# Kernel tuning notes

Measured on AMD Instinct MI355X. Metric: run time of the kernel, lower is better.

The kernel has to match this reference:

```python
import jax, jax.numpy as jnp
import numpy as np

D, NQ, BS, NL, NH, NP, DFF = 256, 900, 8, 4, 8, 4, 1024
HD = D // NH
SHAPES = np.array([[100, 100], [50, 50], [25, 25], [13, 13]], dtype=np.int64)  # (H, W) per level
LSTART = np.concatenate([[0], np.cumsum(SHAPES[:, 0] * SHAPES[:, 1])[:-1]]).astype(np.int64)
LMEM = int((SHAPES[:, 0] * SHAPES[:, 1]).sum())


def layer_norm(x, g, b, eps=1e-5):
    mu = x.mean(-1, keepdims=True)
    var = ((x - mu) ** 2).mean(-1, keepdims=True)
    return (x - mu) * jax.lax.rsqrt(var + eps) * g + b


def _forward(tgt, tgt_query_pos, tgt_reference_points, memory,
             in_proj_w, in_proj_b, out_proj_w, out_proj_b,
             samp_off_w, samp_off_b, attn_w_w, attn_w_b,
             value_proj_w, value_proj_b, output_proj_w, output_proj_b,
             lin1_w, lin1_b, lin2_w, lin2_b,
             norm1_g, norm1_b, norm2_g, norm2_b, norm3_g, norm3_b):
    # ---- self-attention (seq-first, torch nn.MultiheadAttention semantics) ----
    q = tgt + tgt_query_pos  # q = k = with_pos_embed(tgt, pos)
    Wq, Wk, Wv = jnp.split(in_proj_w, 3, 0)
    bq, bk, bv = jnp.split(in_proj_b, 3, 0)
    def heads(x):  # (nq, bs, d) -> (bs, nh, nq, hd)
        return x.reshape(NQ, BS, NH, HD).transpose(1, 2, 0, 3)
    qh = heads(q @ Wq.T + bq)
    kh = heads(q @ Wk.T + bk)
    vh = heads(tgt @ Wv.T + bv)
    attn = jax.nn.softmax(jnp.einsum('bhqd,bhkd->bhqk', qh, kh) / np.float32(np.sqrt(HD)), -1)
    sa = jnp.einsum('bhqk,bhkd->bhqd', attn, vh).transpose(2, 0, 1, 3).reshape(NQ, BS, D)
    sa = sa @ out_proj_w.T + out_proj_b
    t = layer_norm(tgt + sa, norm2_g, norm2_b)

    # ---- MSDeformAttn cross-attention (batch-first internally) ----
    qb = (t + tgt_query_pos).transpose(1, 0, 2)          # (bs, nq, d)
    refb = tgt_reference_points.transpose(1, 0, 2, 3)    # (bs, nq, nl, 2) in [0,1]
    memb = memory.transpose(1, 0, 2)                     # (bs, L, d)
    value = (memb @ value_proj_w.T + value_proj_b).reshape(BS, LMEM, NH, HD)
    off = (qb @ samp_off_w.T + samp_off_b).reshape(BS, NQ, NH, NL, NP, 2)
    aw = jax.nn.softmax((qb @ attn_w_w.T + attn_w_b).reshape(BS, NQ, NH, NL * NP), -1)
    aw = aw.reshape(BS, NQ, NH, NL, NP)
    normz = jnp.asarray(SHAPES[:, ::-1].copy(), dtype=jnp.float32)  # (nl, 2) = [W, H]
    loc = refb[:, :, None, :, None, :] + off / normz[None, None, None, :, None, :]

    out = jnp.zeros((BS, NQ, NH, HD), jnp.float32)
    for l in range(NL):  # fixed small number of pyramid levels
        Hl, Wl = int(SHAPES[l, 0]), int(SHAPES[l, 1])
        s = int(LSTART[l])
        v_l = value[:, s:s + Hl * Wl]  # (bs, Hl*Wl, nh, hd)
        # grid_sample(align_corners=False, padding=zeros) pixel coords
        x = (loc[:, :, :, l, :, 0] * Wl - 0.5).transpose(0, 1, 3, 2).reshape(BS, NQ * NP, NH)
        y = (loc[:, :, :, l, :, 1] * Hl - 0.5).transpose(0, 1, 3, 2).reshape(BS, NQ * NP, NH)
        x0 = jnp.floor(x)
        y0 = jnp.floor(y)
        samp = jnp.zeros((BS, NQ * NP, NH, HD), jnp.float32)
        for dx in (0, 1):
            for dy in (0, 1):
                xc = x0 + dx
                yc = y0 + dy
                w = (1.0 - jnp.abs(x - xc)) * (1.0 - jnp.abs(y - yc))
                valid = (xc >= 0) & (xc < Wl) & (yc >= 0) & (yc < Hl)
                idx = (jnp.clip(yc, 0, Hl - 1) * Wl + jnp.clip(xc, 0, Wl - 1)).astype(jnp.int32)
                g = jnp.take_along_axis(v_l, idx[..., None], axis=1)  # (bs, nq*np, nh, hd)
                samp = samp + jnp.where(valid, w, 0.0)[..., None] * g
        samp = samp.reshape(BS, NQ, NP, NH, HD)
        out = out + jnp.einsum('bqhp,bqphd->bqhd', aw[:, :, :, l], samp)
    ca = (out.reshape(BS, NQ, D) @ output_proj_w.T + output_proj_b).transpose(1, 0, 2)
    t = layer_norm(t + ca, norm1_g, norm1_b)

    # ---- FFN ----
    ffn = jax.nn.relu(t @ lin1_w.T + lin1_b) @ lin2_w.T + lin2_b
    return layer_norm(t + ffn, norm3_g, norm3_b)


def setup_inputs() -> dict:
    key = jax.random.key(0)
    ks = jax.random.split(key, 24)
    r = lambda i, shape, s: jax.random.normal(ks[i], shape, jnp.float32) * s
    return {
        'tgt': r(0, (NQ, BS, D), 1.0),
        'tgt_query_pos': r(1, (NQ, BS, D), 1.0),
        'tgt_reference_points': jax.random.uniform(ks[2], (NQ, BS, NL, 2), jnp.float32),
        'memory': r(3, (LMEM, BS, D), 1.0),
        'spatial_shapes': jnp.asarray(SHAPES),
        'level_start_index': jnp.asarray(LSTART),
        'in_proj_w': r(4, (3 * D, D), 0.02), 'in_proj_b': r(5, (3 * D,), 0.02),
        'out_proj_w': r(6, (D, D), 0.02), 'out_proj_b': r(7, (D,), 0.02),
        'samp_off_w': r(8, (NH * NL * NP * 2, D), 0.01), 'samp_off_b': r(9, (NH * NL * NP * 2,), 0.01),
        'attn_w_w': r(10, (NH * NL * NP, D), 0.02), 'attn_w_b': r(11, (NH * NL * NP,), 0.02),
        'value_proj_w': r(12, (D, D), 0.02), 'value_proj_b': r(13, (D,), 0.02),
        'output_proj_w': r(14, (D, D), 0.02), 'output_proj_b': r(15, (D,), 0.02),
        'lin1_w': r(16, (DFF, D), 0.02), 'lin1_b': r(17, (DFF,), 0.02),
        'lin2_w': r(18, (D, DFF), 0.02), 'lin2_b': r(19, (D,), 0.02),
        'norm1_g': jnp.ones((D,), jnp.float32), 'norm1_b': jnp.zeros((D,), jnp.float32),
        'norm2_g': jnp.ones((D,), jnp.float32), 'norm2_b': jnp.zeros((D,), jnp.float32),
        'norm3_g': jnp.ones((D,), jnp.float32), 'norm3_b': jnp.zeros((D,), jnp.float32),
    }


def reference(tgt, tgt_query_pos, tgt_reference_points, memory, spatial_shapes, level_start_index,
              in_proj_w, in_proj_b, out_proj_w, out_proj_b, samp_off_w, samp_off_b,
              attn_w_w, attn_w_b, value_proj_w, value_proj_b, output_proj_w, output_proj_b,
              lin1_w, lin1_b, lin2_w, lin2_b, norm1_g, norm1_b, norm2_g, norm2_b, norm3_g, norm3_b):
    # spatial_shapes / level_start_index are static level constants (module-level SHAPES/LSTART)
    return _forward(tgt, tgt_query_pos, tgt_reference_points, memory,
                    in_proj_w, in_proj_b, out_proj_w, out_proj_b,
                    samp_off_w, samp_off_b, attn_w_w, attn_w_b,
                    value_proj_w, value_proj_b, output_proj_w, output_proj_b,
                    lin1_w, lin1_b, lin2_w, lin2_b,
                    norm1_g, norm1_b, norm2_g, norm2_b, norm3_g, norm3_b)
```

## Files before the change

kernel.cpp:

```cpp
#include <hip/hip_runtime.h>
#include <hip/hip_bf16.h>


namespace {
constexpr int D_ = 256;
constexpr int NQ_ = 900;
constexpr int BS_ = 8;
constexpr int NH_ = 8;
constexpr int HD_ = 32;
constexpr int DFF_ = 1024;
constexpr int MTOK = NQ_ * BS_;
constexpr int LMEM_ = 13294;
constexpr long T = (long)MTOK * D_;
constexpr float QSC = 0.17677669529663687f;
constexpr int QKS = 512;
constexpr int MVAL = BS_ * LMEM_;
}

typedef __attribute__((ext_vector_type(8))) short bf8_t;
typedef __attribute__((ext_vector_type(4))) float f4_t;

#define MFMA16(a, b, c) __builtin_amdgcn_mfma_f32_16x16x32_bf16((a), (b), (c), 0, 0, 0)

__device__ __forceinline__ unsigned short bfbits(float x) {
    union { __hip_bfloat16 h; unsigned short u; } cv;
    cv.h = __float2bfloat16(x);
    return cv.u;
}
__device__ __forceinline__ float bf2f(unsigned short u) {
    union { float f; unsigned v; } cv;
    cv.v = ((unsigned)u) << 16;
    return cv.f;
}

__device__ __forceinline__ void gload16(const unsigned short* g, unsigned short* l) {
    __builtin_amdgcn_global_load_lds(
        (const __attribute__((address_space(1))) unsigned int*)(g),
        (__attribute__((address_space(3))) unsigned int*)(l), 16, 0, 0);
}
__device__ __forceinline__ void gload16f(const float* g, float* l) {
    __builtin_amdgcn_global_load_lds(
        (const __attribute__((address_space(1))) unsigned int*)(g),
        (__attribute__((address_space(3))) unsigned int*)(l), 16, 0, 0);
}

__global__ void conv_weights(
    const float* __restrict__ ipw, const float* __restrict__ opw,
    const float* __restrict__ sow, const float* __restrict__ aww,
    const float* __restrict__ vpw, const float* __restrict__ outpw,
    const float* __restrict__ l1w, const float* __restrict__ l2w,
    const float* __restrict__ ipb, const float* __restrict__ sob,
    const float* __restrict__ awb,
    unsigned short* __restrict__ Wbf, float* __restrict__ biasAll)
{
    if (blockIdx.x == 0) {
        for (int j = threadIdx.x; j < 512; j += 256)
            biasAll[j] = (j < 256) ? ipb[j] * QSC : ipb[j];
        for (int j = threadIdx.x; j < 384; j += 256)
            biasAll[512 + j] = (j < 256) ? sob[j] : awb[j - 256];
    }
    const long idx4 = (long)blockIdx.x * 256 + threadIdx.x;
    if (idx4 >= 253952) return;
    const long e = idx4 * 4;
    const float* src; long off; float sc = 1.f;
    if (e < 196608)      { src = ipw;   off = 0;      if (e < 65536) sc = QSC; }
    else if (e < 262144) { src = opw;   off = 196608; }
    else if (e < 327680) { src = sow;   off = 262144; }
    else if (e < 360448) { src = aww;   off = 327680; }
    else if (e < 425984) { src = vpw;   off = 360448; }
    else if (e < 491520) { src = outpw; off = 425984; }
    else if (e < 753664) { src = l1w;   off = 491520; }
    else                 { src = l2w;   off = 753664; }
    const float4 v = *(const float4*)(src + (e - off));
    union { unsigned short u[4]; uint2 w; } pk;
    pk.u[0] = bfbits(v.x * sc); pk.u[1] = bfbits(v.y * sc);
    pk.u[2] = bfbits(v.z * sc); pk.u[3] = bfbits(v.w * sc);
    *(uint2*)(Wbf + e) = pk.w;
}

template<bool RELU, bool OUTBF16>
__global__ __launch_bounds__(256) void gemm_mfma(
    const unsigned short* __restrict__ A, const unsigned short* __restrict__ W,
    const float* __restrict__ bias, void* __restrict__ C, int M, int N, int K)
{
    __shared__ unsigned short As[128 * 32];
    __shared__ unsigned short Ws[128 * 32];
    const int t = threadIdx.x;
    const long m0 = (long)blockIdx.x * 128;
    const int n0 = blockIdx.y * 128;
    const int row0 = t >> 2;
    const int cgp = (t & 3) ^ ((t >> 2) & 3);
    long ar0 = m0 + row0;        if (ar0 > M - 1) ar0 = M - 1;
    long ar1 = m0 + 64 + row0;   if (ar1 > M - 1) ar1 = M - 1;
    const unsigned short* ga0 = A + ar0 * K + cgp * 8;
    const unsigned short* ga1 = A + ar1 * K + cgp * 8;
    const unsigned short* gw0 = W + (long)(n0 + row0) * K + cgp * 8;
    const unsigned short* gw1 = W + (long)(n0 + 64 + row0) * K + cgp * 8;
    const int lane = t & 63, wave = t >> 6;
    const int c = lane & 15, g = lane >> 4;
    const int wr = wave >> 1, wc = wave & 1;
    const int sws = (g * 8) ^ ((c & 3) * 8);
    f4_t acc[4][4];
#pragma unroll
    for (int i = 0; i < 4; ++i)
#pragma unroll
        for (int j = 0; j < 4; ++j)
            acc[i][j] = f4_t{0.f, 0.f, 0.f, 0.f};

    for (int kb = 0; kb < K; kb += 32) {
        gload16(ga0 + kb, As + t * 8);
        gload16(ga1 + kb, As + 2048 + t * 8);
        gload16(gw0 + kb, Ws + t * 8);
        gload16(gw1 + kb, Ws + 2048 + t * 8);
        __syncthreads();
        bf8_t af[4], bfr[4];
#pragma unroll
        for (int i = 0; i < 4; ++i) {
            af[i] = *(const bf8_t*)(As + (wr * 64 + i * 16 + c) * 32 + sws);
            bfr[i] = *(const bf8_t*)(Ws + (wc * 64 + i * 16 + c) * 32 + sws);
        }
#pragma unroll
        for (int i = 0; i < 4; ++i)
#pragma unroll
            for (int j = 0; j < 4; ++j)
                acc[i][j] = MFMA16(af[i], bfr[j], acc[i][j]);
        __syncthreads();
    }

#pragma unroll
    for (int i = 0; i < 4; ++i) {
        const long rbase = m0 + wr * 64 + i * 16 + 4 * g;
#pragma unroll
        for (int j = 0; j < 4; ++j) {
            const int col = n0 + wc * 64 + j * 16 + c;
            const float bv = bias[col];
#pragma unroll
            for (int r = 0; r < 4; ++r) {
                const long rr = rbase + r;
                if (rr < M) {
                    float v = acc[i][j][r] + bv;
                    if (RELU) v = fmaxf(v, 0.f);
                    if (OUTBF16) ((unsigned short*)C)[rr * N + col] = bfbits(v);
                    else         ((float*)C)[rr * N + col] = v;
                }
            }
        }
    }
}

template<bool OUTBF16>
__global__ __launch_bounds__(256) void gemm_f32d(
    const float* __restrict__ A, const unsigned short* __restrict__ W,
    const float* __restrict__ bias, void* __restrict__ C,
    int M, int N, int K)
{
    __shared__ float Asf[64 * 64];
    __shared__ unsigned short Ws[128 * 64];
    const int t = threadIdx.x;
    const long m0 = (long)blockIdx.x * 64;
    const int n0 = blockIdx.y * 128;
    const float* gA[4];
#pragma unroll
    for (int l = 0; l < 4; ++l) {
        int r = (int)m0 + l * 16 + (t >> 4); if (r > M - 1) r = M - 1;
        const int sp = (t & 15) ^ ((t >> 4) & 15);
        gA[l] = A + (long)r * K + sp * 4;
    }
    const unsigned short* gW[4];
#pragma unroll
    for (int l = 0; l < 4; ++l) {
        const int r = l * 32 + (t >> 3);
        const int sp = (t & 7) ^ (r & 7);
        gW[l] = W + (long)(n0 + r) * K + sp * 8;
    }
    const int lane = t & 63, wave = t >> 6;
    const int c = lane & 15, g = lane >> 4;
    const int wr = wave >> 1, wc = wave & 1;
    f4_t acc[2][4];
#pragma unroll
    for (int i = 0; i < 2; ++i)
#pragma unroll
        for (int j = 0; j < 4; ++j)
            acc[i][j] = f4_t{0.f, 0.f, 0.f, 0.f};

    for (int kb = 0; kb < K; kb += 64) {
#pragma unroll
        for (int l = 0; l < 4; ++l) gload16f(gA[l] + kb, Asf + l * 1024 + t * 4);
#pragma unroll
        for (int l = 0; l < 4; ++l) gload16(gW[l] + kb, Ws + l * 2048 + t * 8);
        __syncthreads();
#pragma unroll
        for (int s = 0; s < 2; ++s) {
            bf8_t af[2], bfr[4];
#pragma unroll
            for (int i = 0; i < 2; ++i) {
                const int row = wr * 32 + i * 16 + c;
                const int sl0 = (s * 8 + 2 * g) ^ (row & 15);
                const int sl1 = (s * 8 + 2 * g + 1) ^ (row & 15);
                const f4_t lo = *(const f4_t*)(Asf + row * 64 + sl0 * 4);
                const f4_t hi = *(const f4_t*)(Asf + row * 64 + sl1 * 4);
                union { bf8_t v; unsigned short u[8]; } pk;
                pk.u[0] = bfbits(lo[0]); pk.u[1] = bfbits(lo[1]);
                pk.u[2] = bfbits(lo[2]); pk.u[3] = bfbits(lo[3]);
                pk.u[4] = bfbits(hi[0]); pk.u[5] = bfbits(hi[1]);
                pk.u[6] = bfbits(hi[2]); pk.u[7] = bfbits(hi[3]);
                af[i] = pk.v;
            }
#pragma unroll
            for (int j = 0; j < 4; ++j) {
                const int row = wc * 64 + j * 16 + c;
                const int sl = (s * 4 + g) ^ (row & 7);
                bfr[j] = *(const bf8_t*)(Ws + row * 64 + sl * 8);
            }
#pragma unroll
            for (int i = 0; i < 2; ++i)
#pragma unroll
                for (int j = 0; j < 4; ++j)
                    acc[i][j] = MFMA16(af[i], bfr[j], acc[i][j]);
        }
        __syncthreads();
    }

#pragma unroll
    for (int i = 0; i < 2; ++i) {
        const long rbase = m0 + wr * 32 + i * 16 + 4 * g;
#pragma unroll
        for (int j = 0; j < 4; ++j) {
            const int col = n0 + wc * 64 + j * 16 + c;
            const float bv = bias[col];
#pragma unroll
            for (int r = 0; r < 4; ++r) {
                const long rr = rbase + r;
                if (rr < M) {
                    float v = acc[i][j][r] + bv;
                    if (OUTBF16) ((unsigned short*)C)[rr * N + col] = bfbits(v);
                    else         ((float*)C)[rr * N + col] = v;
                }
            }
        }
    }
}

template<bool OUTBF16>
__global__ __launch_bounds__(256) void gemm_f32a(
    const float* __restrict__ A, const float* __restrict__ A2,
    const unsigned short* __restrict__ W, const float* __restrict__ bias,
    void* __restrict__ C, int M, int N, int K)
{
    __shared__ unsigned short As[128 * 32];
    __shared__ unsigned short Ws[128 * 32];
    const int t = threadIdx.x;
    const long m0 = (long)blockIdx.x * 128;
    const int n0 = blockIdx.y * 128;
    const int row0 = t >> 2, cg = t & 3;
    const int cgp = cg ^ ((t >> 2) & 3);
    long ar0 = m0 + row0;        if (ar0 > M - 1) ar0 = M - 1;
    long ar1 = m0 + 64 + row0;   if (ar1 > M - 1) ar1 = M - 1;
    const float* Ap0 = A + ar0 * K + cg * 8;
    const float* Ap1 = A + ar1 * K + cg * 8;
    const float* Bp0 = A2 + ar0 * K + cg * 8;
    const float* Bp1 = A2 + ar1 * K + cg * 8;
    const unsigned short* gw0 = W + (long)(n0 + row0) * K + cgp * 8;
    const unsigned short* gw1 = W + (long)(n0 + 64 + row0) * K + cgp * 8;
    unsigned short* la0 = As + row0 * 32 + ((cg * 8) ^ ((row0 & 3) * 8));
    unsigned short* la1 = la0 + 2048;
    const int lane = t & 63, wave = t >> 6;
    const int c = lane & 15, g = lane >> 4;
    const int wr = wave >> 1, wc = wave & 1;
    const int sws = (g * 8) ^ ((c & 3) * 8);
    f4_t acc[4][4];
#pragma unroll
    for (int i = 0; i < 4; ++i)
#pragma unroll
        for (int j = 0; j < 4; ++j)
            acc[i][j] = f4_t{0.f, 0.f, 0.f, 0.f};

    for (int kb = 0; kb < K; kb += 32) {
        gload16(gw0 + kb, Ws + t * 8);
        gload16(gw1 + kb, Ws + 2048 + t * 8);
        const float4 a00 = *(const float4*)(Ap0 + kb);
        const float4 a01 = *(const float4*)(Ap0 + kb + 4);
        const float4 a10 = *(const float4*)(Ap1 + kb);
        const float4 a11 = *(const float4*)(Ap1 + kb + 4);
        const float4 b00 = *(const float4*)(Bp0 + kb);
        const float4 b01 = *(const float4*)(Bp0 + kb + 4);
        const float4 b10 = *(const float4*)(Bp1 + kb);
        const float4 b11 = *(const float4*)(Bp1 + kb + 4);
        union { bf8_t v; unsigned short u[8]; } p0, p1;
        p0.u[0] = bfbits(a00.x + b00.x); p0.u[1] = bfbits(a00.y + b00.y);
        p0.u[2] = bfbits(a00.z + b00.z); p0.u[3] = bfbits(a00.w + b00.w);
        p0.u[4] = bfbits(a01.x + b01.x); p0.u[5] = bfbits(a01.y + b01.y);
        p0.u[6] = bfbits(a01.z + b01.z); p0.u[7] = bfbits(a01.w + b01.w);
        p1.u[0] = bfbits(a10.x + b10.x); p1.u[1] = bfbits(a10.y + b10.y);
        p1.u[2] = bfbits(a10.z + b10.z); p1.u[3] = bfbits(a10.w + b10.w);
        p1.u[4] = bfbits(a11.x + b11.x); p1.u[5] = bfbits(a11.y + b11.y);
        p1.u[6] = bfbits(a11.z + b11.z); p1.u[7] = bfbits(a11.w + b11.w);
        *(bf8_t*)la0 = p0.v;
        *(bf8_t*)la1 = p1.v;
        __syncthreads();
        bf8_t af[4], bfr[4];
#pragma unroll
        for (int i = 0; i < 4; ++i) {
            af[i] = *(const bf8_t*)(As + (wr * 64 + i * 16 + c) * 32 + sws);
            bfr[i] = *(const bf8_t*)(Ws + (wc * 64 + i * 16 + c) * 32 + sws);
        }
#pragma unroll
        for (int i = 0; i < 4; ++i)
#pragma unroll
            for (int j = 0; j < 4; ++j)
                acc[i][j] = MFMA16(af[i], bfr[j], acc[i][j]);
        __syncthreads();
    }

#pragma unroll
    for (int i = 0; i < 4; ++i) {
        const long rbase = m0 + wr * 64 + i * 16 + 4 * g;
#pragma unroll
        for (int j = 0; j < 4; ++j) {
            const int col = n0 + wc * 64 + j * 16 + c;
            const float bv = bias[col];
#pragma unroll
            for (int r = 0; r < 4; ++r) {
                const long rr = rbase + r;
                if (rr < M) {
                    float v = acc[i][j][r] + bv;
                    if (OUTBF16) ((unsigned short*)C)[rr * N + col] = bfbits(v);
                    else         ((float*)C)[rr * N + col] = v;
                }
            }
        }
    }
}

__global__ __launch_bounds__(256) void attn_mfma(
    const unsigned short* __restrict__ Qb, const unsigned short* __restrict__ Kb,
    const unsigned short* __restrict__ Vb, unsigned short* __restrict__ sa)
{
    __shared__ float smemf[2112];
    unsigned short* Ks = (unsigned short*)smemf;
    unsigned short* Vt = (unsigned short*)(smemf + 1024);
    const int t = threadIdx.x;
    const int wave = t >> 6, lane = t & 63;
    const int g = lane >> 4, c = lane & 15;
    const int b = blockIdx.x >> 3, h = blockIdx.x & 7;
    const int q0 = blockIdx.y * 64 + wave * 16;
    const int q = q0 + c;
    const bool qv = q < NQ_;
    const bf8_t qf = *(const bf8_t*)(Qb + ((long)(qv ? q : 0) * BS_ + b) * QKS + h * HD_ + 8 * g);

    f4_t acc0 = {0.f, 0.f, 0.f, 0.f}, acc1 = {0.f, 0.f, 0.f, 0.f};
    float m_run = -1e30f, l_run = 0.f;
    const int sk = t >> 2, sd = (t & 3) * 8;

    for (int kc = 0; kc < NQ_; kc += 64) {
        __syncthreads();
        {
            const int key = kc + sk;
            union { bf8_t v; unsigned short u[8]; } kv, vv;
            if (key < NQ_) {
                kv.v = *(const bf8_t*)(Kb + ((long)key * BS_ + b) * QKS + h * HD_ + sd);
                vv.v = *(const bf8_t*)(Vb + ((long)key * BS_ + b) * D_ + h * HD_ + sd);
            } else {
#pragma unroll
                for (int u = 0; u < 8; ++u) { kv.u[u] = 0; vv.u[u] = 0; }
            }
            *(bf8_t*)(Ks + sk * 32 + sd) = kv.v;
#pragma unroll
            for (int u = 0; u < 8; ++u) {
                const int r = sd + u;
                Vt[r * 64 + (sk ^ ((r & 7) << 3))] = vv.u[u];
            }
        }
        __syncthreads();

        f4_t s[4];
#pragma unroll
        for (int tt = 0; tt < 4; ++tt) {
            const bf8_t kf = *(const bf8_t*)(Ks + (tt * 16 + c) * 32 + 8 * g);
            f4_t z = {0.f, 0.f, 0.f, 0.f};
            s[tt] = MFMA16(kf, qf, z);
        }
        float sv[16];
#pragma unroll
        for (int tt = 0; tt < 4; ++tt)
#pragma unroll
            for (int r = 0; r < 4; ++r) {
                float x = s[tt][r];
                if (kc + tt * 16 + 4 * g + r >= NQ_) x = -1e30f;
                sv[tt * 4 + r] = x;
            }
        float mloc = sv[0];
#pragma unroll
        for (int i = 1; i < 16; ++i) mloc = fmaxf(mloc, sv[i]);
        mloc = fmaxf(mloc, __shfl_xor(mloc, 16));
        mloc = fmaxf(mloc, __shfl_xor(mloc, 32));
        const float mnew = fmaxf(m_run, mloc);
        const float resc = __expf(m_run - mnew);
        float p[16], ls = 0.f;
#pragma unroll
        for (int i = 0; i < 16; ++i) { p[i] = __expf(sv[i] - mnew); ls += p[i]; }
        ls += __shfl_xor(ls, 16);
        ls += __shfl_xor(ls, 32);
        l_run = l_run * resc + ls;
        m_run = mnew;
#pragma unroll
        for (int r = 0; r < 4; ++r) { acc0[r] *= resc; acc1[r] *= resc; }

        unsigned pk[4][2];
#pragma unroll
        for (int tt = 0; tt < 4; ++tt) {
            pk[tt][0] = (unsigned)bfbits(p[tt * 4 + 0]) | ((unsigned)bfbits(p[tt * 4 + 1]) << 16);
            pk[tt][1] = (unsigned)bfbits(p[tt * 4 + 2]) | ((unsigned)bfbits(p[tt * 4 + 3]) << 16);
        }
        const int srcA = ((g & 1) << 5) + c;
        const int srcB = srcA + 16;
#pragma unroll
        for (int kh = 0; kh < 2; ++kh) {
            const unsigned a0 = __shfl(pk[kh * 2][0], srcA), b0_ = __shfl(pk[kh * 2 + 1][0], srcA);
            const unsigned a1 = __shfl(pk[kh * 2][1], srcA), b1_ = __shfl(pk[kh * 2 + 1][1], srcA);
            const unsigned a2 = __shfl(pk[kh * 2][0], srcB), b2_ = __shfl(pk[kh * 2 + 1][0], srcB);
            const unsigned a3 = __shfl(pk[kh * 2][1], srcB), b3_ = __shfl(pk[kh * 2 + 1][1], srcB);
            union { bf8_t v; unsigned u[4]; } pf;
            const bool hi = (g & 2);
            pf.u[0] = hi ? b0_ : a0; pf.u[1] = hi ? b1_ : a1;
            pf.u[2] = hi ? b2_ : a2; pf.u[3] = hi ? b3_ : a3;
            const int kcol = (kh * 32 + 8 * g) ^ ((c & 7) << 3);
            const bf8_t vf0 = *(const bf8_t*)(Vt + c * 64 + kcol);
            const bf8_t vf1 = *(const bf8_t*)(Vt + (16 + c) * 64 + kcol);
            acc0 = MFMA16(vf0, pf.v, acc0);
            acc1 = MFMA16(vf1, pf.v, acc1);
        }
    }

    __syncthreads();
    const float invl = 1.f / l_run;
    float* O = smemf + wave * 528;
#pragma unroll
    for (int r = 0; r < 4; ++r) {
        O[c * 33 + 4 * g + r] = acc0[r] * invl;
        O[c * 33 + 16 + 4 * g + r] = acc1[r] * invl;
    }
    __syncthreads();
    {
        const int ql = lane >> 2, part = lane & 3;
        const int qg = q0 + ql;
        if (qg < NQ_) {
            union { bf8_t v; unsigned short u[8]; } pk;
#pragma unroll
            for (int u = 0; u < 8; ++u) pk.u[u] = bfbits(O[ql * 33 + part * 8 + u]);
            *(bf8_t*)(sa + ((long)qg * BS_ + b) * D_ + h * HD_ + part * 8) = pk.v;
        }
    }
}

__global__ __launch_bounds__(256) void msdeform_kernel(
    const float* __restrict__ oa, const float* __restrict__ refp,
    const unsigned short* __restrict__ val, unsigned short* __restrict__ out)
{
    __shared__ float saw[128];
    __shared__ float redm[8], redi[8];
    __shared__ float swt[128][4];
    __shared__ int sidx[128][4];
    const int bq = blockIdx.x;
    const int b = bq / NQ_, q = bq % NQ_;
    const int t = threadIdx.x;
    if (t < 128) saw[t] = oa[(long)bq * 384 + 256 + t];
    __syncthreads();
    if (t < 8) {
        float mx = -1e30f;
        for (int i = 0; i < 16; ++i) mx = fmaxf(mx, saw[t * 16 + i]);
        float s = 0.f;
        for (int i = 0; i < 16; ++i) s += __expf(saw[t * 16 + i] - mx);
        redm[t] = mx; redi[t] = 1.f / s;
    }
    __syncthreads();
    if (t < 128) {
        const int h = t >> 4, lp = t & 15, l = lp >> 2, p = lp & 3;
        const float aw = __expf(saw[t] - redm[h]) * redi[h];
        const int Wi = (l == 0) ? 100 : (l == 1) ? 50 : (l == 2) ? 25 : 13;
        const int Hi = Wi;
        const int sl = (l == 0) ? 0 : (l == 1) ? 10000 : (l == 2) ? 12500 : 13125;
        const float offx = oa[(long)bq * 384 + h * 32 + l * 8 + p * 2 + 0];
        const float offy = oa[(long)bq * 384 + h * 32 + l * 8 + p * 2 + 1];
        const float refx = refp[(((long)q * BS_ + b) * 4 + l) * 2 + 0];
        const float refy = refp[(((long)q * BS_ + b) * 4 + l) * 2 + 1];
        const float fW = (float)Wi, fH = (float)Hi;
        const float x = (refx + offx / fW) * fW - 0.5f;
        const float y = (refy + offy / fH) * fH - 0.5f;
        const float x0f = floorf(x), y0f = floorf(y);
        const float fx = x - x0f, fy = y - y0f;
        const int ix = (int)x0f, iy = (int)y0f;
        const float wts[4] = {(1.f - fx) * (1.f - fy), fx * (1.f - fy),
                              (1.f - fx) * fy,          fx * fy};
        const int xs[4] = {ix, ix + 1, ix, ix + 1};
        const int ys[4] = {iy, iy, iy + 1, iy + 1};
#pragma unroll
        for (int tap = 0; tap < 4; ++tap) {
            const bool valid = (xs[tap] >= 0) & (xs[tap] < Wi) & (ys[tap] >= 0) & (ys[tap] < Hi);
            const int xc = min(max(xs[tap], 0), Wi - 1);
            const int yc = min(max(ys[tap], 0), Hi - 1);
            swt[t][tap] = valid ? aw * wts[tap] : 0.f;
            sidx[t][tap] = ((sl + yc * Wi + xc) << 3) + b;
        }
    }
    __syncthreads();
    const int h = t >> 5, r = t & 31, qd = r & 7, s = r >> 3;
    float a0 = 0.f, a1 = 0.f, a2 = 0.f, a3 = 0.f;
#pragma unroll
    for (int i = 0; i < 16; ++i) {
        const int j = h * 16 + i;
        const float wv = swt[j][s];
        const long base = (long)sidx[j][s] * D_ + h * HD_ + qd * 4;
        const uint2 raw = *(const uint2*)(val + base);
        a0 += wv * bf2f((unsigned short)(raw.x & 0xffff));
        a1 += wv * bf2f((unsigned short)(raw.x >> 16));
        a2 += wv * bf2f((unsigned short)(raw.y & 0xffff));
        a3 += wv * bf2f((unsigned short)(raw.y >> 16));
    }
    a0 += __shfl_xor(a0, 8); a0 += __shfl_xor(a0, 16);
    a1 += __shfl_xor(a1, 8); a1 += __shfl_xor(a1, 16);
    a2 += __shfl_xor(a2, 8); a2 += __shfl_xor(a2, 16);
    a3 += __shfl_xor(a3, 8); a3 += __shfl_xor(a3, 16);
    if (s == 0) {
        union { unsigned short u[4]; uint2 w; } pk;
        pk.u[0] = bfbits(a0); pk.u[1] = bfbits(a1); pk.u[2] = bfbits(a2); pk.u[3] = bfbits(a3);
        *(uint2*)(out + (long)bq * D_ + h * HD_ + qd * 4) = pk.w;
    }
}

__global__ __launch_bounds__(256) void ln_kernel(
    const float* __restrict__ inA, const float* __restrict__ inB,
    const float* __restrict__ g, const float* __restrict__ be,
    float* __restrict__ out, const float* __restrict__ pos,
    unsigned short* __restrict__ bfOut, int swapB, int bfMode)
{
    const int r = blockIdx.x * 4 + (threadIdx.x >> 6);
    const int lane = threadIdx.x & 63;
    long rb = r;
    if (swapB) rb = (long)(r & 7) * NQ_ + (r >> 3);
    const float4 a4 = *(const float4*)(inA + (long)r * D_ + lane * 4);
    const float4 b4 = *(const float4*)(inB + rb * D_ + lane * 4);
    float x[4] = {a4.x + b4.x, a4.y + b4.y, a4.z + b4.z, a4.w + b4.w};
    float s = x[0] + x[1] + x[2] + x[3];
#pragma unroll
    for (int off = 32; off > 0; off >>= 1) s += __shfl_xor(s, off);
    const float mu = s * (1.f / D_);
    float v = 0.f;
#pragma unroll
    for (int cc = 0; cc < 4; ++cc) { const float dd = x[cc] - mu; v += dd * dd; }
#pragma unroll
    for (int off = 32; off > 0; off >>= 1) v += __shfl_xor(v, off);
    const float rs = rsqrtf(v * (1.f / D_) + 1e-5f);
    const float4 g4 = *(const float4*)(g + lane * 4);
    const float4 e4 = *(const float4*)(be + lane * 4);
    const float gg[4] = {g4.x, g4.y, g4.z, g4.w};
    const float ee[4] = {e4.x, e4.y, e4.z, e4.w};
    float y[4];
#pragma unroll
    for (int cc = 0; cc < 4; ++cc) y[cc] = (x[cc] - mu) * rs * gg[cc] + ee[cc];
    *(float4*)(out + (long)r * D_ + lane * 4) = make_float4(y[0], y[1], y[2], y[3]);
    if (bfMode) {
        float z[4] = {y[0], y[1], y[2], y[3]};
        long er = r;
        if (bfMode == 2) {
            const float4 p4 = *(const float4*)(pos + (long)r * D_ + lane * 4);
            z[0] += p4.x; z[1] += p4.y; z[2] += p4.z; z[3] += p4.w;
            er = (long)(r & 7) * NQ_ + (r >> 3);
        }
        union { unsigned short u[4]; uint2 w; } pk;
        pk.u[0] = bfbits(z[0]); pk.u[1] = bfbits(z[1]);
        pk.u[2] = bfbits(z[2]); pk.u[3] = bfbits(z[3]);
        *(uint2*)(bfOut + er * D_ + lane * 4) = pk.w;
    }
}

extern "C" void kernel_launch(void* const* d_in, const int* in_sizes, int n_in,
                              void* d_out, int out_size, void* d_ws, size_t ws_size,
                              hipStream_t stream) {
    const float* tgt   = (const float*)d_in[0];
    const float* pos   = (const float*)d_in[1];
    const float* refp  = (const float*)d_in[2];
    const float* mem   = (const float*)d_in[3];
    const float* ipw   = (const float*)d_in[6];
    const float* ipb   = (const float*)d_in[7];
    const float* opw   = (const float*)d_in[8];
    const float* opb   = (const float*)d_in[9];
    const float* sow   = (const float*)d_in[10];
    const float* sob   = (const float*)d_in[11];
    const float* aww   = (const float*)d_in[12];
    const float* awb   = (const float*)d_in[13];
    const float* vpw   = (const float*)d_in[14];
    const float* vpb   = (const float*)d_in[15];
    const float* outpw = (const float*)d_in[16];
    const float* outpb = (const float*)d_in[17];
    const float* l1w   = (const float*)d_in[18];
    const float* l1b   = (const float*)d_in[19];
    const float* l2w   = (const float*)d_in[20];
    const float* l2b   = (const float*)d_in[21];
    const float* n1g = (const float*)d_in[22]; const float* n1be = (const float*)d_in[23];
    const float* n2g = (const float*)d_in[24]; const float* n2be = (const float*)d_in[25];
    const float* n3g = (const float*)d_in[26]; const float* n3be = (const float*)d_in[27];

    char* wsb = (char*)d_ws;
    auto alloc = [&](size_t bytes) { char* p = wsb; wsb += (bytes + 255) & ~(size_t)255; return p; };
    unsigned short* Wbf       = (unsigned short*)alloc(1015808 * 2);
    float*          biasAll   = (float*)alloc(896 * 4);
    unsigned short* QK_bf     = (unsigned short*)alloc(T * 4);
    unsigned short* Vb_bf     = (unsigned short*)alloc(T * 2);
    unsigned short* sa_bf     = (unsigned short*)alloc(T * 2);
    float*          saproj    = (float*)alloc(T * 4);
    float*          t1        = (float*)alloc(T * 4);
    unsigned short* qplus2_bf = (unsigned short*)alloc(T * 2);
    float*          oa        = (float*)alloc((long)MTOK * 384 * 4);
    unsigned short* sampo_bf  = (unsigned short*)alloc(T * 2);
    float*          ca        = (float*)alloc(T * 4);
    float*          t2        = (float*)alloc(T * 4);
    unsigned short* t2_bf     = (unsigned short*)alloc(T * 2);
    unsigned short* ffnh_bf   = (unsigned short*)alloc((long)MTOK * DFF_ * 2);
    float*          ffno      = (float*)alloc(T * 4);
    unsigned short* val       = (unsigned short*)alloc((long)MVAL * D_ * 2);
    const unsigned short* wqk   = Wbf + 0;
    const unsigned short* wv    = Wbf + 131072;
    const unsigned short* wo    = Wbf + 196608;
    const unsigned short* wsoaw = Wbf + 262144;
    const unsigned short* wvp   = Wbf + 360448;
    const unsigned short* wop   = Wbf + 425984;
    const unsigned short* wl1   = Wbf + 491520;
    const unsigned short* wl2   = Wbf + 753664;
    const float* bias_qk = biasAll;
    const float* bias_oa = biasAll + 512;

    const dim3 blk(256);
    const dim3 g_m(57, 2);

    conv_weights<<<992, blk, 0, stream>>>(ipw, opw, sow, aww, vpw, outpw, l1w, l2w,
                                          ipb, sob, awb, Wbf, biasAll);
    gemm_f32a<true><<<dim3(57, 4), blk, 0, stream>>>(tgt, pos, wqk, bias_qk, QK_bf,
                                                     MTOK, QKS, D_);
    gemm_f32d<true><<<dim3(113, 2), blk, 0, stream>>>(tgt, wv, ipb + 2 * D_, Vb_bf,
                                                      MTOK, D_, D_);
    attn_mfma<<<dim3(64, 15), blk, 0, stream>>>(QK_bf, QK_bf + 256, Vb_bf, sa_bf);
    gemm_mfma<false, false><<<g_m, blk, 0, stream>>>(sa_bf, wo, opb, saproj, MTOK, D_, D_);
    ln_kernel<<<1800, blk, 0, stream>>>(tgt, saproj, n2g, n2be, t1, pos, qplus2_bf, 0, 2);
    gemm_f32d<true><<<dim3(1662, 2), blk, 0, stream>>>(mem, wvp, vpb, val,
                                                       MVAL, D_, D_);
    gemm_mfma<false, false><<<dim3(57, 3), blk, 0, stream>>>(qplus2_bf, wsoaw, bias_oa, oa, MTOK, 384, D_);
    msdeform_kernel<<<7200, blk, 0, stream>>>(oa, refp, val, sampo_bf);
    gemm_mfma<false, false><<<g_m, blk, 0, stream>>>(sampo_bf, wop, outpb, ca, MTOK, D_, D_);
    ln_kernel<<<1800, blk, 0, stream>>>(t1, ca, n1g, n1be, t2, nullptr, t2_bf, 1, 1);
    gemm_mfma<true, true><<<dim3(57, 8), blk, 0, stream>>>(t2_bf, wl1, l1b, ffnh_bf, MTOK, DFF_, D_);
    gemm_mfma<false, false><<<g_m, blk, 0, stream>>>(ffnh_bf, wl2, l2b, ffno, MTOK, D_, DFF_);
    ln_kernel<<<1800, blk, 0, stream>>>(t2, ffno, n3g, n3be, (float*)d_out, nullptr, nullptr, 0, 0);
}
```

Measured before the change: 251.1 us.

## Fuse QKV projection into one GEMM and use persistent value-proj GEMM

The Q/K and V in-projections now run as one GEMM over a 768-wide output. A per-block flag skips the pos-embedding add for the V columns, so one launch replaces two and attention reads V from the shared QKV buffer. The memory value projection is replaced by a persistent kernel. It keeps the full 128x256 weight tile resident in LDS, loops over row tiles with a grid-stride loop, and reads fp32 activations straight from global memory into registers instead of staging them through LDS. The trade-off is a large LDS footprint per block (64KB), which limits occupancy, plus uncoalesced direct A loads.

```diff
diff --git a/kernel.cpp b/kernel.cpp
--- a/kernel.cpp
+++ b/kernel.cpp
@@ -13,7 +13,7 @@
 constexpr int LMEM_ = 13294;
 constexpr long T = (long)MTOK * D_;
 constexpr float QSC = 0.17677669529663687f;
-constexpr int QKS = 512;
+constexpr int QKVS = 768;
 constexpr int MVAL = BS_ * LMEM_;
 }
 
@@ -54,10 +54,10 @@
     unsigned short* __restrict__ Wbf, float* __restrict__ biasAll)
 {
     if (blockIdx.x == 0) {
-        for (int j = threadIdx.x; j < 512; j += 256)
+        for (int j = threadIdx.x; j < 768; j += 256)
             biasAll[j] = (j < 256) ? ipb[j] * QSC : ipb[j];
         for (int j = threadIdx.x; j < 384; j += 256)
-            biasAll[512 + j] = (j < 256) ? sob[j] : awb[j - 256];
+            biasAll[768 + j] = (j < 256) ? sob[j] : awb[j - 256];
     }
     const long idx4 = (long)blockIdx.x * 256 + threadIdx.x;
     if (idx4 >= 253952) return;
@@ -148,93 +148,75 @@
     }
 }
 
-template<bool OUTBF16>
-__global__ __launch_bounds__(256) void gemm_f32d(
+__global__ __launch_bounds__(256) void gemm_vdir(
     const float* __restrict__ A, const unsigned short* __restrict__ W,
-    const float* __restrict__ bias, void* __restrict__ C,
-    int M, int N, int K)
+    const float* __restrict__ bias, unsigned short* __restrict__ C)
 {
-    __shared__ float Asf[64 * 64];
-    __shared__ unsigned short Ws[128 * 64];
+    __shared__ unsigned short Wl[128 * 256];
     const int t = threadIdx.x;
-    const long m0 = (long)blockIdx.x * 64;
     const int n0 = blockIdx.y * 128;
-    const float* gA[4];
-#pragma unroll
-    for (int l = 0; l < 4; ++l) {
-        int r = (int)m0 + l * 16 + (t >> 4); if (r > M - 1) r = M - 1;
-        const int sp = (t & 15) ^ ((t >> 4) & 15);
-        gA[l] = A + (long)r * K + sp * 4;
-    }
-    const unsigned short* gW[4];
-#pragma unroll
-    for (int l = 0; l < 4; ++l) {
-        const int r = l * 32 + (t >> 3);
-        const int sp = (t & 7) ^ (r & 7);
-        gW[l] = W + (long)(n0 + r) * K + sp * 8;
-    }
+    {
+        const int rsub = t >> 5, slot = t & 31;
+#pragma unroll
+        for (int i = 0; i < 16; ++i) {
+            const int r = i * 8 + rsub;
+            const int cg = slot ^ (r & 31);
+            gload16(W + (long)(n0 + r) * 256 + cg * 8, Wl + r * 256 + slot * 8);
+        }
+    }
+    __syncthreads();
     const int lane = t & 63, wave = t >> 6;
     const int c = lane & 15, g = lane >> 4;
     const int wr = wave >> 1, wc = wave & 1;
-    f4_t acc[2][4];
-#pragma unroll
-    for (int i = 0; i < 2; ++i)
-#pragma unroll
-        for (int j = 0; j < 4; ++j)
-            acc[i][j] = f4_t{0.f, 0.f, 0.f, 0.f};
-
-    for (int kb = 0; kb < K; kb += 64) {
-#pragma unroll
-        for (int l = 0; l < 4; ++l) gload16f(gA[l] + kb, Asf + l * 1024 + t * 4);
-#pragma unroll
-        for (int l = 0; l < 4; ++l) gload16(gW[l] + kb, Ws + l * 2048 + t * 8);
-        __syncthreads();
-#pragma unroll
-        for (int s = 0; s < 2; ++s) {
-            bf8_t af[2], bfr[4];
-#pragma unroll
-            for (int i = 0; i < 2; ++i) {
-                const int row = wr * 32 + i * 16 + c;
-                const int sl0 = (s * 8 + 2 * g) ^ (row & 15);
-                const int sl1 = (s * 8 + 2 * g + 1) ^ (row & 15);
-                const f4_t lo = *(const f4_t*)(Asf + row * 64 + sl0 * 4);
-                const f4_t hi = *(const f4_t*)(Asf + row * 64 + sl1 * 4);
-                union { bf8_t v; unsigned short u[8]; } pk;
-                pk.u[0] = bfbits(lo[0]); pk.u[1] = bfbits(lo[1]);
-                pk.u[2] = bfbits(lo[2]); pk.u[3] = bfbits(lo[3]);
-                pk.u[4] = bfbits(hi[0]); pk.u[5] = bfbits(hi[1]);
-                pk.u[6] = bfbits(hi[2]); pk.u[7] = bfbits(hi[3]);
-                af[i] = pk.v;
-            }
+
+    for (int mt = blockIdx.x; mt < 1662; mt += 256) {
+        const long m0 = (long)mt * 64;
+        int r0 = (int)m0 + wr * 32 + c;      if (r0 > MVAL - 1) r0 = MVAL - 1;
+        int r1 = r0 + 16;                    if (r1 > MVAL - 1) r1 = MVAL - 1;
+        const float* pA0 = A + (long)r0 * 256 + g * 8;
+        const float* pA1 = A + (long)r1 * 256 + g * 8;
+        f4_t acc[2][4];
+#pragma unroll
+        for (int i = 0; i < 2; ++i)
+#pragma unroll
+            for (int j = 0; j < 4; ++j)
+                acc[i][j] = f4_t{0.f, 0.f, 0.f, 0.f};
+#pragma unroll
+        for (int kk = 0; kk < 8; ++kk) {
+            const float4 l0 = *(const float4*)(pA0 + kk * 32);
+            const float4 h0 = *(const float4*)(pA0 + kk * 32 + 4);
+            const float4 l1 = *(const float4*)(pA1 + kk * 32);
+            const float4 h1 = *(const float4*)(pA1 + kk * 32 + 4);
+            union { bf8_t v; unsigned short u[8]; } p0, p1;
+            p0.u[0] = bfbits(l0.x); p0.u[1] = bfbits(l0.y); p0.u[2] = bfbits(l0.z); p0.u[3] = bfbits(l0.w);
+            p0.u[4] = bfbits(h0.x); p0.u[5] = bfbits(h0.y); p0.u[6] = bfbits(h0.z); p0.u[7] = bfbits(h0.w);
+            p1.u[0] = bfbits(l1.x); p1.u[1] = bfbits(l1.y); p1.u[2] = bfbits(l1.z); p1.u[3] = bfbits(l1.w);
+            p1.u[4] = bfbits(h1.x); p1.u[5] = bfbits(h1.y); p1.u[6] = bfbits(h1.z); p1.u[7] = bfbits(h1.w);
+            bf8_t bfr[4];
 #pragma unroll
             for (int j = 0; j < 4; ++j) {
                 const int row = wc * 64 + j * 16 + c;
-                const int sl = (s * 4 + g) ^ (row & 7);
-                bfr[j] = *(const bf8_t*)(Ws + row * 64 + sl * 8);
-            }
-#pragma unroll
-            for (int i = 0; i < 2; ++i)
-#pragma unroll
-                for (int j = 0; j < 4; ++j)
-                    acc[i][j] = MFMA16(af[i], bfr[j], acc[i][j]);
-        }
-        __syncthreads();
-    }
-
-#pragma unroll
-    for (int i = 0; i < 2; ++i) {
-        const long rbase = m0 + wr * 32 + i * 16 + 4 * g;
-#pragma unroll
-        for (int j = 0; j < 4; ++j) {
-            const int col = n0 + wc * 64 + j * 16 + c;
-            const float bv = bias[col];
-#pragma unroll
-            for (int r = 0; r < 4; ++r) {
-                const long rr = rbase + r;
-                if (rr < M) {
-                    float v = acc[i][j][r] + bv;
-                    if (OUTBF16) ((unsigned short*)C)[rr * N + col] = bfbits(v);
-                    else         ((float*)C)[rr * N + col] = v;
+                const int sl = (kk * 4 + g) ^ (row & 31);
+                bfr[j] = *(const bf8_t*)(Wl + row * 256 + sl * 8);
+            }
+#pragma unroll
+            for (int j = 0; j < 4; ++j) {
+                acc[0][j] = MFMA16(p0.v, bfr[j], acc[0][j]);
+                acc[1][j] = MFMA16(p1.v, bfr[j], acc[1][j]);
+            }
+        }
+#pragma unroll
+        for (int i = 0; i < 2; ++i) {
+            const long rbase = m0 + wr * 32 + i * 16 + 4 * g;
+#pragma unroll
+            for (int j = 0; j < 4; ++j) {
+                const int col = n0 + wc * 64 + j * 16 + c;
+                const float bv = bias[col];
+#pragma unroll
+                for (int r = 0; r < 4; ++r) {
+                    const long rr = rbase + r;
+                    if (rr < MVAL)
+                        C[rr * 256 + col] = bfbits(acc[i][j][r] + bv);
                 }
             }
         }
@@ -245,13 +227,14 @@
 __global__ __launch_bounds__(256) void gemm_f32a(
     const float* __restrict__ A, const float* __restrict__ A2,
     const unsigned short* __restrict__ W, const float* __restrict__ bias,
-    void* __restrict__ C, int M, int N, int K)
+    void* __restrict__ C, int M, int N, int K, int addLim)
 {
     __shared__ unsigned short As[128 * 32];
     __shared__ unsigned short Ws[128 * 32];
     const int t = threadIdx.x;
     const long m0 = (long)blockIdx.x * 128;
     const int n0 = blockIdx.y * 128;
+    const bool useAdd = n0 < addLim;
     const int row0 = t >> 2, cg = t & 3;
     const int cgp = cg ^ ((t >> 2) & 3);
     long ar0 = m0 + row0;        if (ar0 > M - 1) ar0 = M - 1;
@@ -278,23 +261,25 @@
     for (int kb = 0; kb < K; kb += 32) {
         gload16(gw0 + kb, Ws + t * 8);
         gload16(gw1 + kb, Ws + 2048 + t * 8);
-        const float4 a00 = *(const float4*)(Ap0 + kb);
-        const float4 a01 = *(const float4*)(Ap0 + kb + 4);
-        const float4 a10 = *(const float4*)(Ap1 + kb);
-        const float4 a11 = *(const float4*)(Ap1 + kb + 4);
-        const float4 b00 = *(const float4*)(Bp0 + kb);
-        const float4 b01 = *(const float4*)(Bp0 + kb + 4);
-        const float4 b10 = *(const float4*)(Bp1 + kb);
-        const float4 b11 = *(const float4*)(Bp1 + kb + 4);
+        float4 a00 = *(const float4*)(Ap0 + kb);
+        float4 a01 = *(const float4*)(Ap0 + kb + 4);
+        float4 a10 = *(const float4*)(Ap1 + kb);
+        float4 a11 = *(const float4*)(Ap1 + kb + 4);
+        if (useAdd) {
+            const float4 b00 = *(const float4*)(Bp0 + kb);
+            const float4 b01 = *(const float4*)(Bp0 + kb + 4);
+            const float4 b10 = *(const float4*)(Bp1 + kb);
+            const float4 b11 = *(const float4*)(Bp1 + kb + 4);
+            a00.x += b00.x; a00.y += b00.y; a00.z += b00.z; a00.w += b00.w;
+            a01.x += b01.x; a01.y += b01.y; a01.z += b01.z; a01.w += b01.w;
+            a10.x += b10.x; a10.y += b10.y; a10.z += b10.z; a10.w += b10.w;
+            a11.x += b11.x; a11.y += b11.y; a11.z += b11.z; a11.w += b11.w;
+        }
         union { bf8_t v; unsigned short u[8]; } p0, p1;
-        p0.u[0] = bfbits(a00.x + b00.x); p0.u[1] = bfbits(a00.y + b00.y);
-        p0.u[2] = bfbits(a00.z + b00.z); p0.u[3] = bfbits(a00.w + b00.w);
-        p0.u[4] = bfbits(a01.x + b01.x); p0.u[5] = bfbits(a01.y + b01.y);
-        p0.u[6] = bfbits(a01.z + b01.z); p0.u[7] = bfbits(a01.w + b01.w);
-        p1.u[0] = bfbits(a10.x + b10.x); p1.u[1] = bfbits(a10.y + b10.y);
-        p1.u[2] = bfbits(a10.z + b10.z); p1.u[3] = bfbits(a10.w + b10.w);
-        p1.u[4] = bfbits(a11.x + b11.x); p1.u[5] = bfbits(a11.y + b11.y);
-        p1.u[6] = bfbits(a11.z + b11.z); p1.u[7] = bfbits(a11.w + b11.w);
+        p0.u[0] = bfbits(a00.x); p0.u[1] = bfbits(a00.y); p0.u[2] = bfbits(a00.z); p0.u[3] = bfbits(a00.w);
+        p0.u[4] = bfbits(a01.x); p0.u[5] = bfbits(a01.y); p0.u[6] = bfbits(a01.z); p0.u[7] = bfbits(a01.w);
+        p1.u[0] = bfbits(a10.x); p1.u[1] = bfbits(a10.y); p1.u[2] = bfbits(a10.z); p1.u[3] = bfbits(a10.w);
+        p1.u[4] = bfbits(a11.x); p1.u[5] = bfbits(a11.y); p1.u[6] = bfbits(a11.z); p1.u[7] = bfbits(a11.w);
         *(bf8_t*)la0 = p0.v;
         *(bf8_t*)la1 = p1.v;
         __syncthreads();
@@ -346,7 +331,7 @@
     const int q0 = blockIdx.y * 64 + wave * 16;
     const int q = q0 + c;
     const bool qv = q < NQ_;
-    const bf8_t qf = *(const bf8_t*)(Qb + ((long)(qv ? q : 0) * BS_ + b) * QKS + h * HD_ + 8 * g);
+    const bf8_t qf = *(const bf8_t*)(Qb + ((long)(qv ? q : 0) * BS_ + b) * QKVS + h * HD_ + 8 * g);
 
     f4_t acc0 = {0.f, 0.f, 0.f, 0.f}, acc1 = {0.f, 0.f, 0.f, 0.f};
     float m_run = -1e30f, l_run = 0.f;
@@ -358,8 +343,8 @@
             const int key = kc + sk;
             union { bf8_t v; unsigned short u[8]; } kv, vv;
             if (key < NQ_) {
-                kv.v = *(const bf8_t*)(Kb + ((long)key * BS_ + b) * QKS + h * HD_ + sd);
-                vv.v = *(const bf8_t*)(Vb + ((long)key * BS_ + b) * D_ + h * HD_ + sd);
+                kv.v = *(const bf8_t*)(Kb + ((long)key * BS_ + b) * QKVS + h * HD_ + sd);
+                vv.v = *(const bf8_t*)(Vb + ((long)key * BS_ + b) * QKVS + h * HD_ + sd);
             } else {
 #pragma unroll
                 for (int u = 0; u < 8; ++u) { kv.u[u] = 0; vv.u[u] = 0; }
@@ -604,9 +589,8 @@
     char* wsb = (char*)d_ws;
     auto alloc = [&](size_t bytes) { char* p = wsb; wsb += (bytes + 255) & ~(size_t)255; return p; };
     unsigned short* Wbf       = (unsigned short*)alloc(1015808 * 2);
-    float*          biasAll   = (float*)alloc(896 * 4);
-    unsigned short* QK_bf     = (unsigned short*)alloc(T * 4);
-    unsigned short* Vb_bf     = (unsigned short*)alloc(T * 2);
+    float*          biasAll   = (float*)alloc(1152 * 4);
+    unsigned short* QKV_bf    = (unsigned short*)alloc((long)MTOK * QKVS * 2);
     unsigned short* sa_bf     = (unsigned short*)alloc(T * 2);
     float*          saproj    = (float*)alloc(T * 4);
     float*          t1        = (float*)alloc(T * 4);
@@ -619,31 +603,27 @@
     unsigned short* ffnh_bf   = (unsigned short*)alloc((long)MTOK * DFF_ * 2);
     float*          ffno      = (float*)alloc(T * 4);
     unsigned short* val       = (unsigned short*)alloc((long)MVAL * D_ * 2);
-    const unsigned short* wqk   = Wbf + 0;
-    const unsigned short* wv    = Wbf + 131072;
+    const unsigned short* wqkv  = Wbf + 0;
     const unsigned short* wo    = Wbf + 196608;
     const unsigned short* wsoaw = Wbf + 262144;
     const unsigned short* wvp   = Wbf + 360448;
     const unsigned short* wop   = Wbf + 425984;
     const unsigned short* wl1   = Wbf + 491520;
     const unsigned short* wl2   = Wbf + 753664;
-    const float* bias_qk = biasAll;
-    const float* bias_oa = biasAll + 512;
+    const float* bias_qkv = biasAll;
+    const float* bias_oa  = biasAll + 768;
 
     const dim3 blk(256);
     const dim3 g_m(57, 2);
 
     conv_weights<<<992, blk, 0, stream>>>(ipw, opw, sow, aww, vpw, outpw, l1w, l2w,
                                           ipb, sob, awb, Wbf, biasAll);
-    gemm_f32a<true><<<dim3(57, 4), blk, 0, stream>>>(tgt, pos, wqk, bias_qk, QK_bf,
-                                                     MTOK, QKS, D_);
-    gemm_f32d<true><<<dim3(113, 2), blk, 0, stream>>>(tgt, wv, ipb + 2 * D_, Vb_bf,
-                                                      MTOK, D_, D_);
-    attn_mfma<<<dim3(64, 15), blk, 0, stream>>>(QK_bf, QK_bf + 256, Vb_bf, sa_bf);
+    gemm_f32a<true><<<dim3(57, 6), blk, 0, stream>>>(tgt, pos, wqkv, bias_qkv, QKV_bf,
+                                                     MTOK, QKVS, D_, 512);
+    attn_mfma<<<dim3(64, 15), blk, 0, stream>>>(QKV_bf, QKV_bf + 256, QKV_bf + 512, sa_bf);
     gemm_mfma<false, false><<<g_m, blk, 0, stream>>>(sa_bf, wo, opb, saproj, MTOK, D_, D_);
     ln_kernel<<<1800, blk, 0, stream>>>(tgt, saproj, n2g, n2be, t1, pos, qplus2_bf, 0, 2);
-    gemm_f32d<true><<<dim3(1662, 2), blk, 0, stream>>>(mem, wvp, vpb, val,
-                                                       MVAL, D_, D_);
+    gemm_vdir<<<dim3(256, 2), blk, 0, stream>>>(mem, wvp, vpb, val);
     gemm_mfma<false, false><<<dim3(57, 3), blk, 0, stream>>>(qplus2_bf, wsoaw, bias_oa, oa, MTOK, 384, D_);
     msdeform_kernel<<<7200, blk, 0, stream>>>(oa, refp, val, sampo_bf);
     gemm_mfma<false, false><<<g_m, blk, 0, stream>>>(sampo_bf, wop, outpb, ca, MTOK, D_, D_);
```

New measurement: 266.3 us. 6.0% more time.

## Fuse Q/K/V projections into one GEMM and stage value-proj output through LDS

Applied to the files above, without the earlier changes.

The V projection is merged into the Q/K projection GEMM by widening the output to 768 columns. Column blocks past 512 skip adding the positional embedding, so the separate gemm_f32d launch for V goes away, and the attention kernel reads K and V from the interleaved QKV buffer with the wider stride. Separately, the memory value-projection GEMM now writes its bf16 tile into shared memory first and stores it with coalesced 16-byte rows, replacing scattered 2-byte stores. The risk is extra LDS round-trip time and a sync in the epilogue, plus a wider V stride in attention.

```diff
diff --git a/kernel.cpp b/kernel.cpp
--- a/kernel.cpp
+++ b/kernel.cpp
@@ -13,7 +13,7 @@
 constexpr int LMEM_ = 13294;
 constexpr long T = (long)MTOK * D_;
 constexpr float QSC = 0.17677669529663687f;
-constexpr int QKS = 512;
+constexpr int QKVS = 768;
 constexpr int MVAL = BS_ * LMEM_;
 }
 
@@ -54,10 +54,10 @@
     unsigned short* __restrict__ Wbf, float* __restrict__ biasAll)
 {
     if (blockIdx.x == 0) {
-        for (int j = threadIdx.x; j < 512; j += 256)
+        for (int j = threadIdx.x; j < 768; j += 256)
             biasAll[j] = (j < 256) ? ipb[j] * QSC : ipb[j];
         for (int j = threadIdx.x; j < 384; j += 256)
-            biasAll[512 + j] = (j < 256) ? sob[j] : awb[j - 256];
+            biasAll[768 + j] = (j < 256) ? sob[j] : awb[j - 256];
     }
     const long idx4 = (long)blockIdx.x * 256 + threadIdx.x;
     if (idx4 >= 253952) return;
@@ -148,10 +148,9 @@
     }
 }
 
-template<bool OUTBF16>
 __global__ __launch_bounds__(256) void gemm_f32d(
     const float* __restrict__ A, const unsigned short* __restrict__ W,
-    const float* __restrict__ bias, void* __restrict__ C,
+    const float* __restrict__ bias, unsigned short* __restrict__ C,
     int M, int N, int K)
 {
     __shared__ float Asf[64 * 64];
@@ -221,22 +220,27 @@
         __syncthreads();
     }
 
+    unsigned short* Cl = (unsigned short*)Asf;
 #pragma unroll
     for (int i = 0; i < 2; ++i) {
-        const long rbase = m0 + wr * 32 + i * 16 + 4 * g;
+        const int rloc = wr * 32 + i * 16 + 4 * g;
 #pragma unroll
         for (int j = 0; j < 4; ++j) {
-            const int col = n0 + wc * 64 + j * 16 + c;
-            const float bv = bias[col];
-#pragma unroll
-            for (int r = 0; r < 4; ++r) {
-                const long rr = rbase + r;
-                if (rr < M) {
-                    float v = acc[i][j][r] + bv;
-                    if (OUTBF16) ((unsigned short*)C)[rr * N + col] = bfbits(v);
-                    else         ((float*)C)[rr * N + col] = v;
-                }
-            }
+            const int col = wc * 64 + j * 16 + c;
+            const float bv = bias[n0 + col];
+#pragma unroll
+            for (int r = 0; r < 4; ++r)
+                Cl[(rloc + r) * 128 + col] = bfbits(acc[i][j][r] + bv);
+        }
+    }
+    __syncthreads();
+    {
+        const int row = t >> 2, seg = t & 3;
+        const long rr = m0 + row;
+        if (rr < M) {
+            const uint4* src = (const uint4*)(Cl + row * 128 + seg * 32);
+            uint4* dst = (uint4*)(C + rr * N + n0 + seg * 32);
+            dst[0] = src[0]; dst[1] = src[1]; dst[2] = src[2]; dst[3] = src[3];
         }
     }
 }
@@ -245,13 +249,14 @@
 __global__ __launch_bounds__(256) void gemm_f32a(
     const float* __restrict__ A, const float* __restrict__ A2,
     const unsigned short* __restrict__ W, const float* __restrict__ bias,
-    void* __restrict__ C, int M, int N, int K)
+    void* __restrict__ C, int M, int N, int K, int addLim)
 {
     __shared__ unsigned short As[128 * 32];
     __shared__ unsigned short Ws[128 * 32];
     const int t = threadIdx.x;
     const long m0 = (long)blockIdx.x * 128;
     const int n0 = blockIdx.y * 128;
+    const bool useAdd = n0 < addLim;
     const int row0 = t >> 2, cg = t & 3;
     const int cgp = cg ^ ((t >> 2) & 3);
     long ar0 = m0 + row0;        if (ar0 > M - 1) ar0 = M - 1;
@@ -278,23 +283,25 @@
     for (int kb = 0; kb < K; kb += 32) {
         gload16(gw0 + kb, Ws + t * 8);
         gload16(gw1 + kb, Ws + 2048 + t * 8);
-        const float4 a00 = *(const float4*)(Ap0 + kb);
-        const float4 a01 = *(const float4*)(Ap0 + kb + 4);
-        const float4 a10 = *(const float4*)(Ap1 + kb);
-        const float4 a11 = *(const float4*)(Ap1 + kb + 4);
-        const float4 b00 = *(const float4*)(Bp0 + kb);
-        const float4 b01 = *(const float4*)(Bp0 + kb + 4);
-        const float4 b10 = *(const float4*)(Bp1 + kb);
-        const float4 b11 = *(const float4*)(Bp1 + kb + 4);
+        float4 a00 = *(const float4*)(Ap0 + kb);
+        float4 a01 = *(const float4*)(Ap0 + kb + 4);
+        float4 a10 = *(const float4*)(Ap1 + kb);
+        float4 a11 = *(const float4*)(Ap1 + kb + 4);
+        if (useAdd) {
+            const float4 b00 = *(const float4*)(Bp0 + kb);
+            const float4 b01 = *(const float4*)(Bp0 + kb + 4);
+            const float4 b10 = *(const float4*)(Bp1 + kb);
+            const float4 b11 = *(const float4*)(Bp1 + kb + 4);
+            a00.x += b00.x; a00.y += b00.y; a00.z += b00.z; a00.w += b00.w;
+            a01.x += b01.x; a01.y += b01.y; a01.z += b01.z; a01.w += b01.w;
+            a10.x += b10.x; a10.y += b10.y; a10.z += b10.z; a10.w += b10.w;
+            a11.x += b11.x; a11.y += b11.y; a11.z += b11.z; a11.w += b11.w;
+        }
         union { bf8_t v; unsigned short u[8]; } p0, p1;
-        p0.u[0] = bfbits(a00.x + b00.x); p0.u[1] = bfbits(a00.y + b00.y);
-        p0.u[2] = bfbits(a00.z + b00.z); p0.u[3] = bfbits(a00.w + b00.w);
-        p0.u[4] = bfbits(a01.x + b01.x); p0.u[5] = bfbits(a01.y + b01.y);
-        p0.u[6] = bfbits(a01.z + b01.z); p0.u[7] = bfbits(a01.w + b01.w);
-        p1.u[0] = bfbits(a10.x + b10.x); p1.u[1] = bfbits(a10.y + b10.y);
-        p1.u[2] = bfbits(a10.z + b10.z); p1.u[3] = bfbits(a10.w + b10.w);
-        p1.u[4] = bfbits(a11.x + b11.x); p1.u[5] = bfbits(a11.y + b11.y);
-        p1.u[6] = bfbits(a11.z + b11.z); p1.u[7] = bfbits(a11.w + b11.w);
+        p0.u[0] = bfbits(a00.x); p0.u[1] = bfbits(a00.y); p0.u[2] = bfbits(a00.z); p0.u[3] = bfbits(a00.w);
+        p0.u[4] = bfbits(a01.x); p0.u[5] = bfbits(a01.y); p0.u[6] = bfbits(a01.z); p0.u[7] = bfbits(a01.w);
+        p1.u[0] = bfbits(a10.x); p1.u[1] = bfbits(a10.y); p1.u[2] = bfbits(a10.z); p1.u[3] = bfbits(a10.w);
+        p1.u[4] = bfbits(a11.x); p1.u[5] = bfbits(a11.y); p1.u[6] = bfbits(a11.z); p1.u[7] = bfbits(a11.w);
         *(bf8_t*)la0 = p0.v;
         *(bf8_t*)la1 = p1.v;
         __syncthreads();
@@ -346,7 +353,7 @@
     const int q0 = blockIdx.y * 64 + wave * 16;
     const int q = q0 + c;
     const bool qv = q < NQ_;
-    const bf8_t qf = *(const bf8_t*)(Qb + ((long)(qv ? q : 0) * BS_ + b) * QKS + h * HD_ + 8 * g);
+    const bf8_t qf = *(const bf8_t*)(Qb + ((long)(qv ? q : 0) * BS_ + b) * QKVS + h * HD_ + 8 * g);
 
     f4_t acc0 = {0.f, 0.f, 0.f, 0.f}, acc1 = {0.f, 0.f, 0.f, 0.f};
     float m_run = -1e30f, l_run = 0.f;
@@ -358,8 +365,8 @@
             const int key = kc + sk;
             union { bf8_t v; unsigned short u[8]; } kv, vv;
             if (key < NQ_) {
-                kv.v = *(const bf8_t*)(Kb + ((long)key * BS_ + b) * QKS + h * HD_ + sd);
-                vv.v = *(const bf8_t*)(Vb + ((long)key * BS_ + b) * D_ + h * HD_ + sd);
+                kv.v = *(const bf8_t*)(Kb + ((long)key * BS_ + b) * QKVS + h * HD_ + sd);
+                vv.v = *(const bf8_t*)(Vb + ((long)key * BS_ + b) * QKVS + h * HD_ + sd);
             } else {
 #pragma unroll
                 for (int u = 0; u < 8; ++u) { kv.u[u] = 0; vv.u[u] = 0; }
@@ -604,9 +611,8 @@
     char* wsb = (char*)d_ws;
     auto alloc = [&](size_t bytes) { char* p = wsb; wsb += (bytes + 255) & ~(size_t)255; return p; };
     unsigned short* Wbf       = (unsigned short*)alloc(1015808 * 2);
-    float*          biasAll   = (float*)alloc(896 * 4);
-    unsigned short* QK_bf     = (unsigned short*)alloc(T * 4);
-    unsigned short* Vb_bf     = (unsigned short*)alloc(T * 2);
+    float*          biasAll   = (float*)alloc(1152 * 4);
+    unsigned short* QKV_bf    = (unsigned short*)alloc((long)MTOK * QKVS * 2);
     unsigned short* sa_bf     = (unsigned short*)alloc(T * 2);
     float*          saproj    = (float*)alloc(T * 4);
     float*          t1        = (float*)alloc(T * 4);
@@ -619,31 +625,27 @@
     unsigned short* ffnh_bf   = (unsigned short*)alloc((long)MTOK * DFF_ * 2);
     float*          ffno      = (float*)alloc(T * 4);
     unsigned short* val       = (unsigned short*)alloc((long)MVAL * D_ * 2);
-    const unsigned short* wqk   = Wbf + 0;
-    const unsigned short* wv    = Wbf + 131072;
+    const unsigned short* wqkv  = Wbf + 0;
     const unsigned short* wo    = Wbf + 196608;
     const unsigned short* wsoaw = Wbf + 262144;
     const unsigned short* wvp   = Wbf + 360448;
     const unsigned short* wop   = Wbf + 425984;
     const unsigned short* wl1   = Wbf + 491520;
     const unsigned short* wl2   = Wbf + 753664;
-    const float* bias_qk = biasAll;
-    const float* bias_oa = biasAll + 512;
+    const float* bias_qkv = biasAll;
+    const float* bias_oa  = biasAll + 768;
 
     const dim3 blk(256);
     const dim3 g_m(57, 2);
 
     conv_weights<<<992, blk, 0, stream>>>(ipw, opw, sow, aww, vpw, outpw, l1w, l2w,
                                           ipb, sob, awb, Wbf, biasAll);
-    gemm_f32a<true><<<dim3(57, 4), blk, 0, stream>>>(tgt, pos, wqk, bias_qk, QK_bf,
-                                                     MTOK, QKS, D_);
-    gemm_f32d<true><<<dim3(113, 2), blk, 0, stream>>>(tgt, wv, ipb + 2 * D_, Vb_bf,
-                                                      MTOK, D_, D_);
-    attn_mfma<<<dim3(64, 15), blk, 0, stream>>>(QK_bf, QK_bf + 256, Vb_bf, sa_bf);
+    gemm_f32a<true><<<dim3(57, 6), blk, 0, stream>>>(tgt, pos, wqkv, bias_qkv, QKV_bf,
+                                                     MTOK, QKVS, D_, 512);
+    attn_mfma<<<dim3(64, 15), blk, 0, stream>>>(QKV_bf, QKV_bf + 256, QKV_bf + 512, sa_bf);
     gemm_mfma<false, false><<<g_m, blk, 0, stream>>>(sa_bf, wo, opb, saproj, MTOK, D_, D_);
     ln_kernel<<<1800, blk, 0, stream>>>(tgt, saproj, n2g, n2be, t1, pos, qplus2_bf, 0, 2);
-    gemm_f32d<true><<<dim3(1662, 2), blk, 0, stream>>>(mem, wvp, vpb, val,
-                                                       MVAL, D_, D_);
+    gemm_f32d<<<dim3(1662, 2), blk, 0, stream>>>(mem, wvp, vpb, val, MVAL, D_, D_);
     gemm_mfma<false, false><<<dim3(57, 3), blk, 0, stream>>>(qplus2_bf, wsoaw, bias_oa, oa, MTOK, 384, D_);
     msdeform_kernel<<<7200, blk, 0, stream>>>(oa, refp, val, sampo_bf);
     gemm_mfma<false, false><<<g_m, blk, 0, stream>>>(sampo_bf, wop, outpb, ca, MTOK, D_, D_);
```

Result: faster. 235.8 us, median of 2 (-6.1%).
